# Kernel optimization log

Measured on AMD Instinct MI355X. Metric: run time of the kernel, lower is better.

The kernel has to match this reference:

```python
import jax, jax.numpy as jnp
import numpy as np

N_NODES = 100000
N_EDGES = 8192
DEG = 32                      # nodes per hyperedge
NNZ = N_EDGES * DEG
D_IN = 128
D_HID = 128
D_EDGE = 64
EPS = 1e-5


def _batchnorm(x, g, b):
    # normalize per-feature over the batch (dim 0), as a BatchNorm1d in train mode
    mu = jnp.mean(x, axis=0)
    var = jnp.var(x, axis=0)
    return (x - mu) * jax.lax.rsqrt(var + EPS) * g + b


def _hconv(x, src, eid, w, W, b):
    # hypergraph conv: linear -> node->edge weighted sum -> edge->node weighted sum
    h = x @ W + b                                          # [N, Dout]
    m = jax.ops.segment_sum(w[:, None] * h[src], eid, num_segments=N_EDGES)
    out = jax.ops.segment_sum(w[:, None] * m[eid], src, num_segments=N_NODES)
    return out


def setup_inputs() -> dict:
    key = jax.random.key(0)
    ks = jax.random.split(key, 20)
    src = jax.random.randint(ks[0], (NNZ,), 0, N_NODES)
    eid = jnp.arange(NNZ) // DEG                          # every edge id appears DEG times
    edge_index = jnp.stack([src, eid]).astype(jnp.int64)
    s = lambda k, sh, f: jax.random.normal(k, sh, jnp.float32) * f
    return {
        "x": s(ks[1], (N_NODES, D_IN), 1.0),
        "edge_index": edge_index,
        "edge_weight": jax.random.uniform(ks[2], (NNZ,), jnp.float32),
        "edge_features": s(ks[3], (N_EDGES, D_EDGE), 1.0),
        "adj": jax.random.uniform(ks[4], (N_EDGES, N_EDGES), jnp.float32) / N_EDGES,
        "T": 2,
        "norm1_g": jnp.ones((D_IN,), jnp.float32),
        "norm1_b": jnp.zeros((D_IN,), jnp.float32),
        "norm2_g": jnp.ones((D_EDGE,), jnp.float32),
        "norm2_b": jnp.zeros((D_EDGE,), jnp.float32),
        "W1": s(ks[5], (D_IN, D_HID), 0.05),
        "b1": jnp.zeros((D_HID,), jnp.float32),
        "W2": s(ks[6], (D_HID, D_HID), 0.05),
        "b2": jnp.zeros((D_HID,), jnp.float32),
        "Wn": s(ks[7], (D_HID, D_HID), 0.05),
        "We": s(ks[8], (D_EDGE, D_HID), 0.05),
        "Wg": s(ks[9], (D_HID, D_HID), 0.05),
        "cls_w1": s(ks[10], (D_HID, 16), 0.1),
        "cls_b1": jnp.zeros((16,), jnp.float32),
        "cls_w2": s(ks[11], (16, 2), 0.1),
        "cls_b2": jnp.zeros((2,), jnp.float32),
    }


def reference(x, edge_index, edge_weight, edge_features, adj, T,
              norm1_g, norm1_b, norm2_g, norm2_b,
              W1, b1, W2, b2, Wn, We, Wg,
              cls_w1, cls_b1, cls_w2, cls_b2):
    src, eid = edge_index[0], edge_index[1]
    x = _batchnorm(x, norm1_g, norm1_b)
    x = _hconv(x, src, eid, edge_weight, W1, b1)
    x = _hconv(x, src, eid, edge_weight, W2, b2)
    x = jax.nn.relu(x)
    # aggregate_node_features (mean over nodes incident to each hyperedge) —
    # the per-edge Python loop becomes one fused segment reduce
    s = jax.ops.segment_sum(x[src], eid, num_segments=N_EDGES)           # [E, D]
    cnt = jax.ops.segment_sum(jnp.ones_like(eid, jnp.float32), eid, num_segments=N_EDGES)
    node_features = s / jnp.maximum(cnt, 1.0)[:, None]
    ef = _batchnorm(edge_features, norm2_g, norm2_b)
    # edge-level graph convolution with T propagation steps over edge-edge adj
    h = jax.nn.relu(node_features @ Wn + ef @ We)
    for _ in range(T):
        h = jax.nn.relu(adj @ (h @ Wg))
    # classifier head
    out = jax.nn.relu(h @ cls_w1 + cls_b1) @ cls_w2 + cls_b2             # [E, 2]
    return out
```

## Files before the change

kernel.cpp:

```cpp
#include <hip/hip_runtime.h>

#define N_NODESC 100000
#define N_EDGESC 8192
#define DEGC 32
#define DF 128
#define DEF 64
#define EPSV 1e-5f
#define KSPLIT 4
#define KSLICE (N_EDGESC / KSPLIT)

typedef __attribute__((ext_vector_type(8))) short short8;
typedef __attribute__((ext_vector_type(4))) float f32x4;
typedef __attribute__((ext_vector_type(8))) unsigned short ushort8;

typedef const void __attribute__((address_space(1)))* gptr_t;
typedef void __attribute__((address_space(3)))* lptr_t;

struct EW { int e; float w; };

__device__ __forceinline__ unsigned short f2bf(float x) {
    union { float f; unsigned u; } v; v.f = x;
    unsigned r = v.u + 0x7fffu + ((v.u >> 16) & 1u);
    return (unsigned short)(r >> 16);
}

__global__ __launch_bounds__(256) void fused_pre(const float* __restrict__ x,
                                                 const float* __restrict__ ef,
                                                 const int* __restrict__ src,
                                                 const float* __restrict__ ew,
                                                 const float* __restrict__ adj,
                                                 unsigned short* __restrict__ adjbf,
                                                 float* __restrict__ stats,
                                                 int* __restrict__ cnt,
                                                 EW* __restrict__ ewpk) {
    const int b = blockIdx.x;
    if (b >= 1488) {
        size_t i = (size_t)(b - 1488) * 256 + threadIdx.x;
        const f32x4* p = (const f32x4*)adj + i * 2;
        f32x4 a = p[0], bb = p[1];
        ushort8 r;
        r[0] = f2bf(a[0]); r[1] = f2bf(a[1]); r[2] = f2bf(a[2]); r[3] = f2bf(a[3]);
        r[4] = f2bf(bb[0]); r[5] = f2bf(bb[1]); r[6] = f2bf(bb[2]); r[7] = f2bf(bb[3]);
        *((ushort8*)adjbf + i) = r;
        return;
    }
    if (b >= 464) {
        int i = (b - 464) * 256 + threadIdx.x;
        int n = src[i];
        int pos = atomicAdd(&cnt[n], 1);
        if (pos < DEGC) {
            EW t; t.e = i >> 5; t.w = ew[i];
            ewpk[(size_t)n * DEGC + pos] = t;
        }
        return;
    }
    __shared__ f32x4 ls[256], lq[256];
    if (b < 400) {
        const int q = threadIdx.x & 31, rg = threadIdx.x >> 5;
        f32x4 s = {0.f, 0.f, 0.f, 0.f}, s2 = {0.f, 0.f, 0.f, 0.f};
        for (int r = b * 8 + rg; r < N_NODESC; r += 3200) {
            f32x4 v = *(const f32x4*)&x[(size_t)r * DF + q * 4];
            s += v; s2 += v * v;
        }
        ls[threadIdx.x] = s; lq[threadIdx.x] = s2;
        __syncthreads();
        if (threadIdx.x < 32) {
            #pragma unroll
            for (int g = 1; g < 8; ++g) { s += ls[threadIdx.x + g * 32]; s2 += lq[threadIdx.x + g * 32]; }
            #pragma unroll
            for (int i = 0; i < 4; ++i) {
                atomicAdd(&stats[q * 4 + i], s[i]);
                atomicAdd(&stats[128 + q * 4 + i], s2[i]);
            }
        }
    } else {
        const int bb = b - 400;
        const int q = threadIdx.x & 15, rg = threadIdx.x >> 4;
        f32x4 s = {0.f, 0.f, 0.f, 0.f}, s2 = {0.f, 0.f, 0.f, 0.f};
        for (int r = bb * 16 + rg; r < N_EDGESC; r += 1024) {
            f32x4 v = *(const f32x4*)&ef[(size_t)r * DEF + q * 4];
            s += v; s2 += v * v;
        }
        ls[threadIdx.x] = s; lq[threadIdx.x] = s2;
        __syncthreads();
        if (threadIdx.x < 16) {
            #pragma unroll
            for (int g = 1; g < 16; ++g) { s += ls[threadIdx.x + g * 16]; s2 += lq[threadIdx.x + g * 16]; }
            #pragma unroll
            for (int i = 0; i < 4; ++i) {
                atomicAdd(&stats[512 + q * 4 + i], s[i]);
                atomicAdd(&stats[576 + q * 4 + i], s2[i]);
            }
        }
    }
}

__global__ void finalize_both(const float* __restrict__ stats,
                              const float* __restrict__ g1, const float* __restrict__ b1,
                              const float* __restrict__ g2, const float* __restrict__ b2,
                              float* __restrict__ ssx, float* __restrict__ sse) {
    int t = threadIdx.x;
    if (t < 128) {
        float mean = stats[t] / (float)N_NODESC;
        float var = stats[128 + t] / (float)N_NODESC - mean * mean;
        float sc = g1[t] * rsqrtf(var + EPSV);
        ssx[t] = sc;
        ssx[128 + t] = b1[t] - mean * sc;
    } else {
        int f = t - 128;
        float mean = stats[512 + f] / (float)N_EDGESC;
        float var = stats[576 + f] / (float)N_EDGESC - mean * mean;
        float sc = g2[f] * rsqrtf(var + EPSV);
        sse[f] = sc;
        sse[64 + f] = b2[f] - mean * sc;
    }
}

__global__ __launch_bounds__(256) void node_apply(const float* __restrict__ m,
                                                  const int* __restrict__ cnt,
                                                  const EW* __restrict__ ewpk,
                                                  float* __restrict__ out) {
    const int n = blockIdx.x * 2 + (threadIdx.x >> 7);
    const int f = threadIdx.x & 127;
    if (n >= N_NODESC) return;
    int d = cnt[n];
    if (d <= 0) return;
    d = min(d, DEGC);
    const EW* q = ewpk + (size_t)n * DEGC;
    float acc = 0.f;
    for (int p = 0; p < d; ++p) {
        EW t = q[p];
        acc += t.w * m[(size_t)t.e * DF + f];
    }
    out[(size_t)n * DF + f] = acc;
}

template<bool WEIGHTED, bool AFFINE, bool RELU, bool WRITE_SW>
__global__ __launch_bounds__(128) void gather_k(const float* __restrict__ X,
                                                const float* __restrict__ w,
                                                const int* __restrict__ src,
                                                const float* __restrict__ scale,
                                                const float* __restrict__ shift,
                                                float* __restrict__ out,
                                                float* __restrict__ swout,
                                                float mul) {
    const int e = blockIdx.x, f = threadIdx.x;
    const int base = e * DEGC;
    float acc = 0.f, sw = 0.f;
    #pragma unroll
    for (int j = 0; j < DEGC; ++j) {
        int n = src[base + j];
        float wj = WEIGHTED ? w[base + j] : 1.f;
        float v = X[(size_t)n * DF + f];
        if (RELU) v = fmaxf(v, 0.f);
        acc += wj * v;
        sw += wj;
    }
    float r = acc;
    if (AFFINE) r = acc * scale[f] + sw * shift[f];
    out[(size_t)e * DF + f] = r * mul;
    if (WRITE_SW && f == 0) swout[e] = sw;
}

template<int K1, int K2, int NSLICE, bool RELU_IN, bool RELU_OUT, bool BIAS>
__global__ __launch_bounds__(256) void egemm(const float* __restrict__ A1, const float* __restrict__ W1p,
                                             const float* __restrict__ A2, const float* __restrict__ W2p,
                                             const float* __restrict__ sc2, const float* __restrict__ sh2,
                                             const float* __restrict__ bias, const float* __restrict__ swv,
                                             float* __restrict__ C) {
    constexpr int P1 = K1 + 4;
    constexpr int K2c = (K2 > 0) ? K2 : 1;
    constexpr int P2 = K2c + 4;
    constexpr size_t SLSTR = (size_t)N_EDGESC * K1;
    __shared__ float wt1[DF * P1];
    __shared__ float a1c[32 * K1];
    __shared__ float wt2[(K2 > 0) ? DF * P2 : 1];
    __shared__ float a2c[(K2 > 0) ? 32 * K2c : 1];

    const int tid = threadIdx.x;
    const int r0 = blockIdx.x * 32;

    for (int idx = tid; idx < K1 * DF; idx += 256) {
        int k = idx >> 7, c = idx & 127;
        wt1[c * P1 + k] = W1p[idx];
    }
    for (int idx = tid; idx < 32 * K1; idx += 256) {
        float v;
        if constexpr (NSLICE > 1) {
            v = 0.f;
            #pragma unroll
            for (int s = 0; s < NSLICE; ++s) v += A1[s * SLSTR + (size_t)r0 * K1 + idx];
        } else {
            v = A1[(size_t)r0 * K1 + idx];
        }
        if (RELU_IN) v = fmaxf(v, 0.f);
        a1c[idx] = v;
    }
    if constexpr (K2 > 0) {
        for (int idx = tid; idx < K2 * DF; idx += 256) {
            int k = idx >> 7, c = idx & 127;
            wt2[c * P2 + k] = W2p[idx];
        }
        for (int idx = tid; idx < 32 * K2; idx += 256) {
            int k = idx % K2;
            a2c[idx] = A2[(size_t)r0 * K2 + idx] * sc2[k] + sh2[k];
        }
    }
    __syncthreads();

    const int cg = tid & 31, rg = tid >> 5;
    float acc[4][4];
    if constexpr (BIAS) {
        float bl[4], sl[4];
        #pragma unroll
        for (int j = 0; j < 4; ++j) bl[j] = bias[cg * 4 + j];
        #pragma unroll
        for (int i = 0; i < 4; ++i) sl[i] = swv[r0 + rg * 4 + i];
        #pragma unroll
        for (int i = 0; i < 4; ++i)
            #pragma unroll
            for (int j = 0; j < 4; ++j) acc[i][j] = sl[i] * bl[j];
    } else {
        #pragma unroll
        for (int i = 0; i < 4; ++i)
            #pragma unroll
            for (int j = 0; j < 4; ++j) acc[i][j] = 0.f;
    }

    #pragma unroll 4
    for (int k4 = 0; k4 < K1; k4 += 4) {
        f32x4 av[4], wv[4];
        #pragma unroll
        for (int i = 0; i < 4; ++i) av[i] = *(const f32x4*)&a1c[(rg * 4 + i) * K1 + k4];
        #pragma unroll
        for (int j = 0; j < 4; ++j) wv[j] = *(const f32x4*)&wt1[(cg * 4 + j) * P1 + k4];
        #pragma unroll
        for (int i = 0; i < 4; ++i)
            #pragma unroll
            for (int j = 0; j < 4; ++j)
                #pragma unroll
                for (int q = 0; q < 4; ++q) acc[i][j] += av[i][q] * wv[j][q];
    }
    if constexpr (K2 > 0) {
        #pragma unroll 4
        for (int k4 = 0; k4 < K2; k4 += 4) {
            f32x4 av[4], wv[4];
            #pragma unroll
            for (int i = 0; i < 4; ++i) av[i] = *(const f32x4*)&a2c[(rg * 4 + i) * K2c + k4];
            #pragma unroll
            for (int j = 0; j < 4; ++j) wv[j] = *(const f32x4*)&wt2[(cg * 4 + j) * P2 + k4];
            #pragma unroll
            for (int i = 0; i < 4; ++i)
                #pragma unroll
                for (int j = 0; j < 4; ++j)
                    #pragma unroll
                    for (int q = 0; q < 4; ++q) acc[i][j] += av[i][q] * wv[j][q];
        }
    }

    #pragma unroll
    for (int i = 0; i < 4; ++i) {
        f32x4 o;
        #pragma unroll
        for (int j = 0; j < 4; ++j) {
            float v = acc[i][j];
            if (RELU_OUT) v = fmaxf(v, 0.f);
            o[j] = v;
        }
        *(f32x4*)&C[(size_t)(r0 + rg * 4 + i) * DF + cg * 4] = o;
    }
}

__global__ __launch_bounds__(256) void transp_cvt(const float* __restrict__ Y,
                                                  unsigned short* __restrict__ Yt) {
    __shared__ float t[32][33];
    const int r0 = blockIdx.x * 32, c0 = blockIdx.y * 32;
    const int tc = threadIdx.x & 31, tr = threadIdx.x >> 5;
    #pragma unroll
    for (int i = 0; i < 4; ++i)
        t[tr + i * 8][tc] = Y[(size_t)(r0 + tr + i * 8) * DF + c0 + tc];
    __syncthreads();
    #pragma unroll
    for (int i = 0; i < 4; ++i) {
        int c = tr + i * 8;
        Yt[(size_t)(c0 + c) * N_EDGESC + r0 + tc] = f2bf(t[tc][c]);
    }
}

__global__ __launch_bounds__(256, 2) void adj_gemm(const unsigned short* __restrict__ A,
                                                   const unsigned short* __restrict__ Bt,
                                                   float* __restrict__ H) {
    __shared__ unsigned short sA[2][128 * 64];
    __shared__ unsigned short sB[2][128 * 64];
    const int tid = threadIdx.x;
    const int lane = tid & 63, wave = tid >> 6;
    const int mb = blockIdx.x & 63, ks = blockIdx.x >> 6;
    const size_t m0 = (size_t)mb * 128;
    const int k0 = ks * KSLICE;
    const int wm = wave >> 1, wn = wave & 1;
    float* __restrict__ Hs = H + (size_t)ks * (N_EDGESC * DF);

    f32x4 acc[4][4];
    #pragma unroll
    for (int i = 0; i < 4; ++i)
        #pragma unroll
        for (int j = 0; j < 4; ++j) acc[i][j] = 0.f;

    auto stage = [&](int buf, int kc) {
        #pragma unroll
        for (int i = 0; i < 4; ++i) {
            int slot = i * 256 + wave * 64 + lane;
            int row = slot >> 3, ch = slot & 7;
            int sc = (ch ^ (row & 7)) << 3;
            const unsigned short* ga = A + (m0 + row) * (size_t)N_EDGESC + kc + sc;
            const unsigned short* gb = Bt + (size_t)row * N_EDGESC + kc + sc;
            unsigned short* la = &sA[buf][(i * 256 + wave * 64) * 8];
            unsigned short* lb = &sB[buf][(i * 256 + wave * 64) * 8];
            __builtin_amdgcn_global_load_lds((gptr_t)ga, (lptr_t)la, 16, 0, 0);
            __builtin_amdgcn_global_load_lds((gptr_t)gb, (lptr_t)lb, 16, 0, 0);
        }
    };

    stage(0, k0);
    int cur = 0;
    for (int c = 0; c < KSLICE / 64; ++c) {
        __syncthreads();
        if (c + 1 < KSLICE / 64) stage(cur ^ 1, k0 + (c + 1) * 64);
        #pragma unroll
        for (int kk = 0; kk < 2; ++kk) {
            short8 af[4], bv[4];
            const int chb = kk * 4 + (lane >> 4);
            #pragma unroll
            for (int mf = 0; mf < 4; ++mf) {
                int row = wm * 64 + mf * 16 + (lane & 15);
                af[mf] = *(const short8*)&sA[cur][(row * 8 + (chb ^ (row & 7))) * 8];
            }
            #pragma unroll
            for (int nf = 0; nf < 4; ++nf) {
                int row = wn * 64 + nf * 16 + (lane & 15);
                bv[nf] = *(const short8*)&sB[cur][(row * 8 + (chb ^ (row & 7))) * 8];
            }
            #pragma unroll
            for (int mf = 0; mf < 4; ++mf)
                #pragma unroll
                for (int nf = 0; nf < 4; ++nf)
                    acc[mf][nf] = __builtin_amdgcn_mfma_f32_16x16x32_bf16(af[mf], bv[nf], acc[mf][nf], 0, 0, 0);
        }
        cur ^= 1;
    }

    #pragma unroll
    for (int mf = 0; mf < 4; ++mf)
        #pragma unroll
        for (int nf = 0; nf < 4; ++nf)
            #pragma unroll
            for (int r = 0; r < 4; ++r) {
                size_t row = m0 + wm * 64 + mf * 16 + (lane >> 4) * 4 + r;
                int col = wn * 64 + nf * 16 + (lane & 15);
                Hs[row * DF + col] = acc[mf][nf][r];
            }
}

__global__ __launch_bounds__(256) void classifier_k(const float* __restrict__ H,
                                                    const float* __restrict__ w1, const float* __restrict__ b1,
                                                    const float* __restrict__ w2, const float* __restrict__ b2,
                                                    float* __restrict__ out) {
    constexpr size_t SLSTR = (size_t)N_EDGESC * DF;
    __shared__ float hl[16 * DF];
    __shared__ float w1l[DF * 16];
    __shared__ float hid[16 * 16];
    const int tid = threadIdx.x;
    const int e0 = blockIdx.x * 16;
    for (int idx = tid; idx < 16 * DF; idx += 256) {
        float v = 0.f;
        #pragma unroll
        for (int s = 0; s < KSPLIT; ++s) v += H[s * SLSTR + (size_t)e0 * DF + idx];
        hl[idx] = fmaxf(v, 0.f);
    }
    for (int idx = tid; idx < DF * 16; idx += 256) w1l[idx] = w1[idx];
    __syncthreads();
    {
        int el = tid >> 4, j = tid & 15;
        float a = b1[j];
        for (int k = 0; k < DF; ++k) a += hl[el * DF + k] * w1l[k * 16 + j];
        hid[el * 16 + j] = fmaxf(a, 0.f);
    }
    __syncthreads();
    if (tid < 32) {
        int e = tid >> 1, o = tid & 1;
        float s = b2[o];
        for (int jj = 0; jj < 16; ++jj) s += hid[e * 16 + jj] * w2[jj * 2 + o];
        out[(size_t)(e0 + e) * 2 + o] = s;
    }
}

extern "C" void kernel_launch(void* const* d_in, const int* in_sizes, int n_in,
                              void* d_out, int out_size, void* d_ws, size_t ws_size,
                              hipStream_t stream) {
    const float* x   = (const float*)d_in[0];
    const int*  src  = (const int*)d_in[1];
    const float* ew  = (const float*)d_in[2];
    const float* ef  = (const float*)d_in[3];
    const float* adj = (const float*)d_in[4];
    const float* n1g = (const float*)d_in[6];
    const float* n1b = (const float*)d_in[7];
    const float* n2g = (const float*)d_in[8];
    const float* n2b = (const float*)d_in[9];
    const float* W1  = (const float*)d_in[10];
    const float* b1  = (const float*)d_in[11];
    const float* W2  = (const float*)d_in[12];
    const float* b2  = (const float*)d_in[13];
    const float* Wn  = (const float*)d_in[14];
    const float* We  = (const float*)d_in[15];
    const float* Wg  = (const float*)d_in[16];
    const float* cw1 = (const float*)d_in[17];
    const float* cb1 = (const float*)d_in[18];
    const float* cw2 = (const float*)d_in[19];
    const float* cb2 = (const float*)d_in[20];
    float* out = (float*)d_out;

    float* stats  = (float*)d_ws;
    float* ssx    = stats + 256;
    float* sse    = stats + 640;
    float* sw     = stats + 1024;
    int*   cnt    = (int*)(sw + 8192);
    EW*    ewpk   = (EW*)(cnt + N_NODESC);
    float* EB0    = (float*)(ewpk + (size_t)N_NODESC * DEGC);
    float* EB1    = EB0 + (size_t)N_EDGESC * DF;
    float* HS     = EB1 + (size_t)N_EDGESC * DF;
    float* NODES  = HS + (size_t)KSPLIT * N_EDGESC * DF;
    unsigned short* yT    = (unsigned short*)(NODES + (size_t)N_NODESC * DF);
    unsigned short* adjbf = yT + (size_t)DF * N_EDGESC;

    (void)hipMemsetAsync(stats, 0, (1024 + 8192) * sizeof(float) + N_NODESC * sizeof(int), stream);

    fused_pre<<<1488 + (N_EDGESC * (N_EDGESC / 8)) / 256, 256, 0, stream>>>(
        x, ef, src, ew, adj, adjbf, stats, cnt, ewpk);
    finalize_both<<<1, 192, 0, stream>>>(stats, n1g, n1b, n2g, n2b, ssx, sse);

    gather_k<true, true, false, true><<<N_EDGESC, 128, 0, stream>>>(x, ew, src, ssx, ssx + 128, EB0, sw, 1.f);
    egemm<128, 0, 1, false, false, true><<<256, 256, 0, stream>>>(EB0, W1, nullptr, nullptr, nullptr, nullptr, b1, sw, EB1);
    node_apply<<<N_NODESC / 2, 256, 0, stream>>>(EB1, cnt, ewpk, NODES);

    gather_k<true, false, false, false><<<N_EDGESC, 128, 0, stream>>>(NODES, ew, src, nullptr, nullptr, EB0, nullptr, 1.f);
    egemm<128, 0, 1, false, false, true><<<256, 256, 0, stream>>>(EB0, W2, nullptr, nullptr, nullptr, nullptr, b2, sw, EB1);
    node_apply<<<N_NODESC / 2, 256, 0, stream>>>(EB1, cnt, ewpk, NODES);

    gather_k<false, false, true, false><<<N_EDGESC, 128, 0, stream>>>(NODES, nullptr, src, nullptr, nullptr, EB0, nullptr, 1.f / DEGC);

    egemm<128, 64, 1, false, true, false><<<256, 256, 0, stream>>>(EB0, Wn, ef, We, sse, sse + 64, nullptr, nullptr, EB1);

    egemm<128, 0, 1, false, false, false><<<256, 256, 0, stream>>>(EB1, Wg, nullptr, nullptr, nullptr, nullptr, nullptr, nullptr, EB0);
    transp_cvt<<<dim3(256, 4), 256, 0, stream>>>(EB0, yT);
    adj_gemm<<<64 * KSPLIT, 256, 0, stream>>>(adjbf, yT, HS);
    egemm<128, 0, KSPLIT, true, false, false><<<256, 256, 0, stream>>>(HS, Wg, nullptr, nullptr, nullptr, nullptr, nullptr, nullptr, EB0);
    transp_cvt<<<dim3(256, 4), 256, 0, stream>>>(EB0, yT);
    adj_gemm<<<64 * KSPLIT, 256, 0, stream>>>(adjbf, yT, HS);

    classifier_k<<<N_EDGESC / 16, 256, 0, stream>>>(HS, cw1, cb1, cw2, cb2, out);
}
```

Baseline: 503.5 us.

## Widen adj bf16 conversion, schedule it first, and double adj GEMM k-split

```diff
diff --git a/kernel.cpp b/kernel.cpp
--- a/kernel.cpp
+++ b/kernel.cpp
@@ -6,8 +6,12 @@
 #define DF 128
 #define DEF 64
 #define EPSV 1e-5f
-#define KSPLIT 4
+#define KSPLIT 8
 #define KSLICE (N_EDGESC / KSPLIT)
+
+#define NCVT 16384
+#define NXST 400
+#define NEST 64
 
 typedef __attribute__((ext_vector_type(8))) short short8;
 typedef __attribute__((ext_vector_type(4))) float f32x4;
@@ -22,6 +26,13 @@
     union { float f; unsigned u; } v; v.f = x;
     unsigned r = v.u + 0x7fffu + ((v.u >> 16) & 1u);
     return (unsigned short)(r >> 16);
+}
+
+__device__ __forceinline__ ushort8 cvt8(f32x4 a, f32x4 b) {
+    ushort8 r;
+    r[0] = f2bf(a[0]); r[1] = f2bf(a[1]); r[2] = f2bf(a[2]); r[3] = f2bf(a[3]);
+    r[4] = f2bf(b[0]); r[5] = f2bf(b[1]); r[6] = f2bf(b[2]); r[7] = f2bf(b[3]);
+    return r;
 }
 
 __global__ __launch_bounds__(256) void fused_pre(const float* __restrict__ x,
@@ -34,18 +45,18 @@
                                                  int* __restrict__ cnt,
                                                  EW* __restrict__ ewpk) {
     const int b = blockIdx.x;
-    if (b >= 1488) {
-        size_t i = (size_t)(b - 1488) * 256 + threadIdx.x;
-        const f32x4* p = (const f32x4*)adj + i * 2;
-        f32x4 a = p[0], bb = p[1];
-        ushort8 r;
-        r[0] = f2bf(a[0]); r[1] = f2bf(a[1]); r[2] = f2bf(a[2]); r[3] = f2bf(a[3]);
-        r[4] = f2bf(bb[0]); r[5] = f2bf(bb[1]); r[6] = f2bf(bb[2]); r[7] = f2bf(bb[3]);
-        *((ushort8*)adjbf + i) = r;
+    if (b < NCVT) {
+        size_t i = (size_t)b * 256 + threadIdx.x;
+        const f32x4* p = (const f32x4*)adj + i * 4;
+        f32x4 a0 = p[0], a1 = p[1], a2 = p[2], a3 = p[3];
+        ushort8* o = (ushort8*)adjbf + i * 2;
+        o[0] = cvt8(a0, a1);
+        o[1] = cvt8(a2, a3);
         return;
     }
-    if (b >= 464) {
-        int i = (b - 464) * 256 + threadIdx.x;
+    const int bs = b - NCVT;
+    if (bs >= NXST + NEST) {
+        int i = (bs - NXST - NEST) * 256 + threadIdx.x;
         int n = src[i];
         int pos = atomicAdd(&cnt[n], 1);
         if (pos < DEGC) {
@@ -55,10 +66,10 @@
         return;
     }
     __shared__ f32x4 ls[256], lq[256];
-    if (b < 400) {
+    if (bs < NXST) {
         const int q = threadIdx.x & 31, rg = threadIdx.x >> 5;
         f32x4 s = {0.f, 0.f, 0.f, 0.f}, s2 = {0.f, 0.f, 0.f, 0.f};
-        for (int r = b * 8 + rg; r < N_NODESC; r += 3200) {
+        for (int r = bs * 8 + rg; r < N_NODESC; r += NXST * 8) {
             f32x4 v = *(const f32x4*)&x[(size_t)r * DF + q * 4];
             s += v; s2 += v * v;
         }
@@ -74,10 +85,10 @@
             }
         }
     } else {
-        const int bb = b - 400;
+        const int bb = bs - NXST;
         const int q = threadIdx.x & 15, rg = threadIdx.x >> 4;
         f32x4 s = {0.f, 0.f, 0.f, 0.f}, s2 = {0.f, 0.f, 0.f, 0.f};
-        for (int r = bb * 16 + rg; r < N_EDGESC; r += 1024) {
+        for (int r = bb * 16 + rg; r < N_EDGESC; r += NEST * 16) {
             f32x4 v = *(const f32x4*)&ef[(size_t)r * DEF + q * 4];
             s += v; s2 += v * v;
         }
@@ -434,7 +445,7 @@
 
     (void)hipMemsetAsync(stats, 0, (1024 + 8192) * sizeof(float) + N_NODESC * sizeof(int), stream);
 
-    fused_pre<<<1488 + (N_EDGESC * (N_EDGESC / 8)) / 256, 256, 0, stream>>>(
+    fused_pre<<<NCVT + NXST + NEST + (N_EDGESC * DEGC) / 256, 256, 0, stream>>>(
         x, ef, src, ew, adj, adjbf, stats, cnt, ewpk);
     finalize_both<<<1, 192, 0, stream>>>(stats, n1g, n1b, n2g, n2b, ssx, sse);
 
```

Result: no change. 498.7 us (-1.0%).
